# Kernel optimization log

Hardware: AMD Instinct MI355X
Metric: run time of the kernel (lower is better)

The kernel has to match this reference:

```python
import jax, jax.numpy as jnp
import numpy as np

B, N, D, H, HID = 8, 512, 512, 8, 2048


def setup_inputs() -> dict:
    key = jax.random.key(0)
    ks = jax.random.split(key, 8)
    s = 0.02
    p = lambda i, shape: jax.random.normal(ks[i], shape, jnp.float32) * s
    return dict(
        x=jax.random.normal(ks[0], (B, N, D), jnp.float32),
        Wq=p(1, (D, D)), bq=jnp.zeros((D,), jnp.float32),
        Wk=p(2, (D, D)), bk=jnp.zeros((D,), jnp.float32),
        Wv=p(3, (D, D)), bv=jnp.zeros((D,), jnp.float32),
        Wsig=p(4, (H, D)), bsig=jnp.zeros((H,), jnp.float32),
        ln1_g=jnp.ones((D,), jnp.float32), ln1_b=jnp.zeros((D,), jnp.float32),
        W1=p(5, (HID, D)), b1=jnp.zeros((HID,), jnp.float32),
        W2=p(6, (D, HID)), b2=jnp.zeros((D,), jnp.float32),
        ln2_g=jnp.ones((D,), jnp.float32), ln2_b=jnp.zeros((D,), jnp.float32),
    )


def _ln(z, g, b, eps=1e-5):
    m = jnp.mean(z, axis=-1, keepdims=True)
    v = jnp.var(z, axis=-1, keepdims=True)
    return (z - m) * jax.lax.rsqrt(v + eps) * g + b


def reference(x, Wq, bq, Wk, bk, Wv, bv, Wsig, bsig,
              ln1_g, ln1_b, W1, b1, W2, b2, ln2_g, ln2_b):
    Bb, Nn, Dd = x.shape
    Hh = bsig.shape[0]
    dh = Dd // Hh
    # --- AnomalyAttention: series attention S, Gaussian prior P, Z = S @ V ---
    Q = (x @ Wq.T + bq).reshape(Bb, Nn, Hh, dh)
    K = (x @ Wk.T + bk).reshape(Bb, Nn, Hh, dh)
    V = (x @ Wv.T + bv).reshape(Bb, Nn, Hh, dh)
    scores = jnp.einsum('bnhd,bmhd->bhnm', Q, K) / jnp.sqrt(jnp.float32(dh))
    S = jax.nn.softmax(scores, axis=-1)                       # [B,H,N,N]
    # learned positive scale sigma per (batch, position, head)
    sigma = jax.nn.softplus(x @ Wsig.T + bsig) + 1e-5         # [B,N,H]
    idx = jnp.arange(Nn, dtype=jnp.float32)
    dist2 = (idx[:, None] - idx[None, :]) ** 2                # [N,N]
    sig = jnp.transpose(sigma, (0, 2, 1))[..., None]          # [B,H,N,1]
    gauss = jnp.exp(-dist2 / (2.0 * sig * sig)) / (jnp.sqrt(2.0 * jnp.pi) * sig)
    P = gauss / jnp.sum(gauss, axis=-1, keepdims=True)        # row-normalized prior
    Zh = jnp.einsum('bhnm,bmhd->bnhd', S, V).reshape(Bb, Nn, Dd)
    # --- residual + LayerNorm + MLP(relu) + residual + LayerNorm ---
    Z = _ln(Zh + x, ln1_g, ln1_b)
    hidden = jax.nn.relu(Z @ W1.T + b1)
    x_hat = hidden @ W2.T + b2
    x_hat = _ln(x_hat + Z, ln2_g, ln2_b)
    return (x_hat, P, S)
```

## Files before the change

### kernel.cpp

```cpp
#include <hip/hip_runtime.h>
#include <cstdint>

typedef short s16x8 __attribute__((ext_vector_type(8)));
typedef float f32x4 __attribute__((ext_vector_type(4)));
using u16 = unsigned short;


__device__ __forceinline__ u16 f2bf(float f) {
    union { float f; uint32_t u; } v; v.f = f;
    uint32_t u = v.u;
    return (u16)((u + 0x7FFFu + ((u >> 16) & 1u)) >> 16);
}
__device__ __forceinline__ float bf2f(u16 u) {
    return __uint_as_float(((uint32_t)u) << 16);
}

__device__ __forceinline__ void gload_lds16(const void* g, void* l) {
    __builtin_amdgcn_global_load_lds(
        (const __attribute__((address_space(1))) unsigned int*)g,
        (__attribute__((address_space(3))) unsigned int*)l, 16, 0, 0);
}

__global__ __launch_bounds__(256) void k_convert_sigma(
    const float* __restrict__ x, const float* __restrict__ wq,
    const float* __restrict__ wk, const float* __restrict__ wv,
    const float* __restrict__ w1, const float* __restrict__ w2,
    const float* __restrict__ bq, const float* __restrict__ bk,
    const float* __restrict__ bv,
    const float* __restrict__ Wsig, const float* __restrict__ bsig,
    u16* __restrict__ xb, u16* __restrict__ wqb, u16* __restrict__ wkb,
    u16* __restrict__ wvb, u16* __restrict__ w1b, u16* __restrict__ w2b,
    float* __restrict__ biascat, float* __restrict__ sigT)
{
    int bk_ = blockIdx.x;
    int tid = threadIdx.x;
    if (bk_ >= 4866) {
        int row  = (int)(((bk_ - 4866) * 256 + tid) >> 6);
        int lane = tid & 63;
        const float4* xr = (const float4*)(x + (long)row * 512);
        float4 xa = xr[lane * 2], xc = xr[lane * 2 + 1];
        float xs[8] = {xa.x, xa.y, xa.z, xa.w, xc.x, xc.y, xc.z, xc.w};
        float ph[8];
#pragma unroll
        for (int h = 0; h < 8; ++h) {
            const float4* wr = (const float4*)(Wsig + h * 512);
            float4 wa = wr[lane * 2], wc = wr[lane * 2 + 1];
            ph[h] = xs[0]*wa.x + xs[1]*wa.y + xs[2]*wa.z + xs[3]*wa.w
                  + xs[4]*wc.x + xs[5]*wc.y + xs[6]*wc.z + xs[7]*wc.w;
        }
#pragma unroll
        for (int h = 0; h < 8; ++h)
#pragma unroll
            for (int m = 1; m < 64; m <<= 1)
                ph[h] += __shfl_xor(ph[h], m, 64);
        if (lane < 8) {
            float z  = ph[lane] + bsig[lane];
            float sp = fmaxf(z, 0.f) + log1pf(__expf(-fabsf(z)));
            int b = row >> 9, n = row & 511;
            sigT[(((long)b * 8 + lane) << 9) + n] = sp + 1e-5f;
        }
        return;
    }
    long g = (long)bk_ * 256 + tid;
    if (g >= 1245184) {
        long id = g - 1245184;
        if (id < 384) {
            const float* src = id < 128 ? bq : id < 256 ? bk : bv;
            ((float4*)biascat)[id] = ((const float4*)src)[id & 127];
        }
        return;
    }
    const float* src; u16* dst; long off;
    if      (g <  524288) { src = x;  dst = xb;  off = g; }
    else if (g <  589824) { src = wq; dst = wqb; off = g -  524288; }
    else if (g <  655360) { src = wk; dst = wkb; off = g -  589824; }
    else if (g <  720896) { src = wv; dst = wvb; off = g -  655360; }
    else if (g <  983040) { src = w1; dst = w1b; off = g -  720896; }
    else                  { src = w2; dst = w2b; off = g -  983040; }
    float4 v = ((const float4*)src)[off];
    ushort4 o;
    o.x = f2bf(v.x); o.y = f2bf(v.y); o.z = f2bf(v.z); o.w = f2bf(v.w);
    ((ushort4*)dst)[off] = o;
}

template<int BM, int BN, int EPI>
__device__ __forceinline__ void gemm_body(
    const u16* __restrict__ A, const u16* __restrict__ B,
    const float* __restrict__ bias, void* __restrict__ C,
    int lda, int ldb, int K, int bx, int by,
    u16* __restrict__ As, u16* __restrict__ Bs)
{
    constexpr int BK = 64;
    const u16* Ag = A + (long)bx * BM * lda;
    const u16* Bg = B + (long)by * BN * ldb;

    int tid  = threadIdx.x;
    int wave = tid >> 6, lane = tid & 63;
    int wm = wave >> 2, wn = wave & 3;
    constexpr int WTM = BM / 2, WTN = BN / 4;
    constexpr int FM = WTM / 16, FN = WTN / 16;
    int r16 = lane & 15, g4 = lane >> 4;

    f32x4 acc[FM][FN];
#pragma unroll
    for (int i = 0; i < FM; ++i)
#pragma unroll
        for (int j = 0; j < FN; ++j) acc[i][j] = (f32x4){0.f, 0.f, 0.f, 0.f};

    constexpr int nA = BM * BK / (512 * 8);
    constexpr int nB = BN * BK / (512 * 8);

    auto stage = [&](int buf, int k0) {
#pragma unroll
        for (int c = 0; c < nA; ++c) {
            int e = c * 512 + tid;
            int r = e >> 3, s = e & 7;
            gload_lds16(Ag + (long)r * lda + k0 + ((s ^ (r & 7)) * 8),
                        &As[buf * BM * BK + e * 8]);
        }
#pragma unroll
        for (int c = 0; c < nB; ++c) {
            int e = c * 512 + tid;
            int r = e >> 3, s = e & 7;
            gload_lds16(Bg + (long)r * ldb + k0 + ((s ^ (r & 7)) * 8),
                        &Bs[buf * BN * BK + e * 8]);
        }
    };

    stage(0, 0);
    __syncthreads();
    int cur = 0;
    const int NT = K / BK;
    for (int t = 0; t < NT; ++t) {
        if (t + 1 < NT) stage(cur ^ 1, (t + 1) * BK);
#pragma unroll
        for (int kk = 0; kk < 2; ++kk) {
            s16x8 af[FM], bfr[FN];
#pragma unroll
            for (int fm = 0; fm < FM; ++fm) {
                int row = wm * WTM + fm * 16 + r16;
                int slot = (kk * 4 + g4) ^ (row & 7);
                af[fm] = *(const s16x8*)&As[cur * BM * BK + row * 64 + slot * 8];
            }
#pragma unroll
            for (int fn = 0; fn < FN; ++fn) {
                int row = wn * WTN + fn * 16 + r16;
                int slot = (kk * 4 + g4) ^ (row & 7);
                bfr[fn] = *(const s16x8*)&Bs[cur * BN * BK + row * 64 + slot * 8];
            }
#pragma unroll
            for (int fm = 0; fm < FM; ++fm)
#pragma unroll
                for (int fn = 0; fn < FN; ++fn)
                    acc[fm][fn] = __builtin_amdgcn_mfma_f32_16x16x32_bf16(af[fm], bfr[fn], acc[fm][fn], 0, 0, 0);
        }
        __syncthreads();
        cur ^= 1;
    }

    int i0 = bx * BM + wm * WTM;
    int j0 = by * BN + wn * WTN;
#pragma unroll
    for (int fm = 0; fm < FM; ++fm)
#pragma unroll
        for (int fn = 0; fn < FN; ++fn)
#pragma unroll
            for (int j = 0; j < 4; ++j) {
                int gi = i0 + fm * 16 + (g4 << 2) + j;
                int gj = j0 + fn * 16 + r16;
                float v = acc[fm][fn][j];
                if constexpr (EPI == 3) {
                    v = fmaxf(v + bias[gj], 0.f);
                    ((u16*)C)[(long)gi * 2048 + gj] = f2bf(v);
                } else if constexpr (EPI == 4) {
                    ((float*)C)[(long)gi * 512 + gj] = v + bias[gj];
                } else {
                    v += bias[gj];
                    int mat = gj >> 9, cj = gj & 511;
                    int h = cj >> 6, d = cj & 63, b = gi >> 9, n = gi & 511;
                    u16* base = (u16*)C;
                    if (mat == 0)
                        base[(((long)(b * 8 + h) * 512 + n) << 6) + d] = f2bf(v);
                    else if (mat == 1)
                        (base + 2097152)[(((long)(b * 8 + h) * 512 + n) << 6) + d] = f2bf(v);
                    else
                        (base + 4194304)[(((long)(b * 8 + h) * 64 + d) << 9) + n] = f2bf(v);
                }
            }
}

template<int BM, int BN, int EPI>
__global__ __launch_bounds__(512) void k_gemm_nt(
    const u16* __restrict__ A, const u16* __restrict__ B,
    const float* __restrict__ bias, void* __restrict__ C,
    int lda, int ldb, int K)
{
    __shared__ __align__(16) u16 As[2 * BM * 64];
    __shared__ __align__(16) u16 Bs[2 * BN * 64];
    gemm_body<BM, BN, EPI>(A, B, bias, C, lda, ldb, K,
                           blockIdx.x, blockIdx.y, As, Bs);
}

__global__ __launch_bounds__(256) void k_attn_prior(
    const u16* __restrict__ Qb, const u16* __restrict__ Kb,
    const u16* __restrict__ Vt, const float* __restrict__ sigT,
    float* __restrict__ S, float* __restrict__ Zh, float* __restrict__ P)
{
    __shared__ __align__(16) u16 Sb[4][16][264];
    __shared__ float cmbM[2][2][16];
    __shared__ float cmbS[2][2][16];
    __shared__ float zc[2][16][66];

    int gid = blockIdx.x;
    int tid = threadIdx.x;
    int wave = tid >> 6, lane = tid & 63;

    if (gid % 9 != 0) {
        int pid = gid - gid / 9 - 1;
        int row = pid * 4 + wave;
        int n = row & 511;
        float s = sigT[row];
        float a = -1.0f / (2.0f * s * s);
        float e[8]; float sum = 0.f;
#pragma unroll
        for (int j = 0; j < 8; ++j) {
            float d = (float)(n - (lane * 8 + j));
            e[j] = __expf(a * d * d);
            sum += e[j];
        }
#pragma unroll
        for (int m = 1; m < 64; m <<= 1) sum += __shfl_xor(sum, m, 64);
        float r = 1.0f / sum;
        f32x4* dst = (f32x4*)(P + (long)row * 512 + lane * 8);
        dst[0] = (f32x4){e[0]*r, e[1]*r, e[2]*r, e[3]*r};
        dst[1] = (f32x4){e[4]*r, e[5]*r, e[6]*r, e[7]*r};
        return;
    }

    int aid = gid / 9;
    int bh = aid & 63;
    int rb = aid >> 6;
    int rg = wave >> 1, ch = wave & 1;
    int r16 = lane & 15, g4 = lane >> 4, hi8 = g4 * 8;

    int row0 = rb * 32 + rg * 16;
    const u16* Qg = Qb + ((long)bh * 512 + row0) * 64;
    const u16* Kg = Kb + ((long)bh * 512 + ch * 256) * 64;
    const u16* Vg = Vt + (long)bh * 64 * 512;

    s16x8 qa[2];
    qa[0] = *(const s16x8*)(Qg + r16 * 64 + hi8);
    qa[1] = *(const s16x8*)(Qg + r16 * 64 + 32 + hi8);

    f32x4 acc[16];
#pragma unroll
    for (int t = 0; t < 16; ++t) acc[t] = (f32x4){0.f, 0.f, 0.f, 0.f};

    __builtin_amdgcn_s_setprio(1);
#pragma unroll
    for (int kk = 0; kk < 2; ++kk)
#pragma unroll
        for (int t = 0; t < 16; ++t) {
            s16x8 b = *(const s16x8*)(Kg + (long)(t * 16 + r16) * 64 + kk * 32 + hi8);
            acc[t] = __builtin_amdgcn_mfma_f32_16x16x32_bf16(qa[kk], b, acc[t], 0, 0, 0);
        }
    __builtin_amdgcn_s_setprio(0);

    float mx[4] = {-1e30f, -1e30f, -1e30f, -1e30f};
#pragma unroll
    for (int t = 0; t < 16; ++t)
#pragma unroll
        for (int j = 0; j < 4; ++j) mx[j] = fmaxf(mx[j], acc[t][j]);
#pragma unroll
    for (int j = 0; j < 4; ++j)
#pragma unroll
        for (int m = 1; m < 16; m <<= 1) mx[j] = fmaxf(mx[j], __shfl_xor(mx[j], m, 64));

    float sm[4] = {0.f, 0.f, 0.f, 0.f};
#pragma unroll
    for (int t = 0; t < 16; ++t)
#pragma unroll
        for (int j = 0; j < 4; ++j) {
            float p = __expf(0.125f * (acc[t][j] - mx[j]));
            acc[t][j] = p;
            sm[j] += p;
        }
#pragma unroll
    for (int j = 0; j < 4; ++j)
#pragma unroll
        for (int m = 1; m < 16; m <<= 1) sm[j] += __shfl_xor(sm[j], m, 64);

    if (r16 == 0) {
#pragma unroll
        for (int j = 0; j < 4; ++j) {
            cmbM[rg][ch][g4 * 4 + j] = mx[j];
            cmbS[rg][ch][g4 * 4 + j] = sm[j];
        }
    }
    __syncthreads();

    float scale[4];
#pragma unroll
    for (int j = 0; j < 4; ++j) {
        float mo = cmbM[rg][ch ^ 1][g4 * 4 + j];
        float so = cmbS[rg][ch ^ 1][g4 * 4 + j];
        float M  = fmaxf(mx[j], mo);
        float tot = sm[j] * __expf(mx[j] - M) + so * __expf(mo - M);
        scale[j] = __expf(mx[j] - M) / tot;
    }
#pragma unroll
    for (int t = 0; t < 16; ++t)
#pragma unroll
        for (int j = 0; j < 4; ++j) acc[t][j] *= scale[j];

#pragma unroll
    for (int t = 0; t < 16; ++t)
#pragma unroll
        for (int j = 0; j < 4; ++j)
            Sb[wave][g4 * 4 + j][t * 16 + r16] = f2bf(acc[t][j]);

    f32x4 zacc[4];
#pragma unroll
    for (int fn = 0; fn < 4; ++fn) zacc[fn] = (f32x4){0.f, 0.f, 0.f, 0.f};

    __builtin_amdgcn_s_setprio(1);
#pragma unroll
    for (int kb = 0; kb < 8; ++kb) {
        s16x8 pa = *(const s16x8*)&Sb[wave][r16][kb * 32 + hi8];
#pragma unroll
        for (int fn = 0; fn < 4; ++fn) {
            s16x8 vb = *(const s16x8*)(Vg + (long)(fn * 16 + r16) * 512 + ch * 256 + kb * 32 + hi8);
            zacc[fn] = __builtin_amdgcn_mfma_f32_16x16x32_bf16(pa, vb, zacc[fn], 0, 0, 0);
        }
    }
    __builtin_amdgcn_s_setprio(0);

    long sbase = ((long)bh * 512 + row0) * 512 + ch * 256;
#pragma unroll
    for (int r = 0; r < 16; ++r) {
        ushort4 u = *(const ushort4*)&Sb[wave][r][lane * 4];
        *(f32x4*)&S[sbase + (long)r * 512 + lane * 4] =
            (f32x4){bf2f(u.x), bf2f(u.y), bf2f(u.z), bf2f(u.w)};
    }

    if (ch == 1) {
#pragma unroll
        for (int fn = 0; fn < 4; ++fn)
#pragma unroll
            for (int j = 0; j < 4; ++j)
                zc[rg][g4 * 4 + j][fn * 16 + r16] = zacc[fn][j];
    }
    __syncthreads();
    if (ch == 0) {
        long zb = ((long)(bh >> 3) * 512 + row0) * 512 + (bh & 7) * 64;
#pragma unroll
        for (int fn = 0; fn < 4; ++fn)
#pragma unroll
            for (int j = 0; j < 4; ++j)
                Zh[zb + (long)(g4 * 4 + j) * 512 + fn * 16 + r16] =
                    zacc[fn][j] + zc[rg][g4 * 4 + j][fn * 16 + r16];
    }
}

template<bool WBF>
__global__ __launch_bounds__(256) void k_ln(
    const float* __restrict__ a, const float* __restrict__ b,
    const float* __restrict__ g, const float* __restrict__ bt,
    float* __restrict__ y, u16* __restrict__ yb)
{
    int row  = (int)((blockIdx.x * 256 + threadIdx.x) >> 6);
    int lane = threadIdx.x & 63;
    const float4* ar = (const float4*)(a + (long)row * 512);
    const float4* br = (const float4*)(b + (long)row * 512);
    float4 a0 = ar[lane * 2], a1 = ar[lane * 2 + 1];
    float4 b0 = br[lane * 2], b1 = br[lane * 2 + 1];
    float v[8] = {a0.x + b0.x, a0.y + b0.y, a0.z + b0.z, a0.w + b0.w,
                  a1.x + b1.x, a1.y + b1.y, a1.z + b1.z, a1.w + b1.w};
    float s = 0.f, q = 0.f;
#pragma unroll
    for (int j = 0; j < 8; ++j) { s += v[j]; q += v[j] * v[j]; }
#pragma unroll
    for (int m = 1; m < 64; m <<= 1) {
        s += __shfl_xor(s, m, 64);
        q += __shfl_xor(q, m, 64);
    }
    float mean = s * (1.f / 512.f);
    float var  = q * (1.f / 512.f) - mean * mean;
    float rstd = rsqrtf(var + 1e-5f);
    const float4* gr = (const float4*)(g + lane * 8);
    const float4* tr = (const float4*)(bt + lane * 8);
    float4 g0 = gr[0], g1 = gr[1], t0 = tr[0], t1 = tr[1];
    float gg[8] = {g0.x, g0.y, g0.z, g0.w, g1.x, g1.y, g1.z, g1.w};
    float tt[8] = {t0.x, t0.y, t0.z, t0.w, t1.x, t1.y, t1.z, t1.w};
    float o[8];
#pragma unroll
    for (int j = 0; j < 8; ++j) o[j] = (v[j] - mean) * rstd * gg[j] + tt[j];
    float4* yr = (float4*)(y + (long)row * 512 + lane * 8);
    yr[0] = make_float4(o[0], o[1], o[2], o[3]);
    yr[1] = make_float4(o[4], o[5], o[6], o[7]);
    if constexpr (WBF) {
        s16x8 ob;
#pragma unroll
        for (int j = 0; j < 8; ++j) ob[j] = (short)f2bf(o[j]);
        *(s16x8*)(yb + (long)row * 512 + lane * 8) = ob;
    }
}

extern "C" void kernel_launch(void* const* d_in, const int* in_sizes, int n_in,
                              void* d_out, int out_size, void* d_ws, size_t ws_size,
                              hipStream_t stream)
{
    const float* x    = (const float*)d_in[0];
    const float* Wq   = (const float*)d_in[1];
    const float* bq   = (const float*)d_in[2];
    const float* Wk   = (const float*)d_in[3];
    const float* bk   = (const float*)d_in[4];
    const float* Wv   = (const float*)d_in[5];
    const float* bv   = (const float*)d_in[6];
    const float* Wsig = (const float*)d_in[7];
    const float* bsig = (const float*)d_in[8];
    const float* g1   = (const float*)d_in[9];
    const float* be1  = (const float*)d_in[10];
    const float* W1   = (const float*)d_in[11];
    const float* b1   = (const float*)d_in[12];
    const float* W2   = (const float*)d_in[13];
    const float* b2   = (const float*)d_in[14];
    const float* g2   = (const float*)d_in[15];
    const float* be2  = (const float*)d_in[16];

    float* out_xhat = (float*)d_out;
    float* out_P    = out_xhat + 2097152;
    float* out_S    = out_P + 16777216;

    char* ws = (char*)d_ws;
    u16*   xb   = (u16*)(ws + 0);
    u16*   Qb   = (u16*)(ws + 4194304);
    u16*   hid  = (u16*)(ws + 0);
    u16*   Wqb  = (u16*)(ws + 16777216);
    u16*   W1b  = (u16*)(ws + 18350080);
    u16*   W2b  = (u16*)(ws + 20447232);
    float* sigT = (float*)(ws + 22544384);
    float* Zh   = (float*)(ws + 22675456);
    float* bcat = (float*)(ws + 22675456);
    float* x2   = (float*)(ws + 22675456);
    float* Z    = (float*)(ws + 31064064);
    u16*   Zb   = (u16*)(ws + 39452672);

    u16* Wkb = Wqb + 262144;
    u16* Wvb = Wqb + 524288;

    k_convert_sigma<<<5890, 256, 0, stream>>>(x, Wq, Wk, Wv, W1, W2, bq, bk, bv,
                                              Wsig, bsig,
                                              xb, Wqb, Wkb, Wvb, W1b, W2b,
                                              bcat, sigT);

    k_gemm_nt<128,128,5><<<dim3(32,12,1),512,0,stream>>>(
        xb, Wqb, bcat, Qb, 512, 512, 512);

    k_attn_prior<<<9216, 256, 0, stream>>>(Qb, Qb + 2097152, Qb + 4194304,
                                           sigT, out_S, Zh, out_P);

    k_ln<true><<<1024,256,0,stream>>>(Zh, x, g1, be1, Z, Zb);

    k_gemm_nt<128,128,3><<<dim3(32,16,1),512,0,stream>>>(Zb, W1b, b1, hid, 512, 512, 512);

    k_gemm_nt<64,128,4><<<dim3(64,4,1),512,0,stream>>>(hid, W2b, b2, x2, 2048, 2048, 2048);

    k_ln<false><<<1024,256,0,stream>>>(x2, Z, g2, be2, out_xhat, nullptr);
}
```

Measured before the change: 142.2 us.

## Split Gaussian prior work between QKV GEMM launch and attention kernel

Half of the Gaussian prior rows are now computed by extra blocks appended to the QKV projection GEMM launch, with the other half still in the attention kernel. The attention kernel's grid shrinks and uses a simpler block-to-work mapping. The S write-back is moved before the S·V MFMA loop. The intent is to overlap memory-bound prior writes with the compute-bound GEMM and to rebalance the attention launch, at the cost of a larger combined kernel whose 512-thread prior blocks also carry the GEMM's LDS footprint.

New measurement: 133.8 us, median of 2. -5.9%, faster.

```diff
diff --git a/kernel.cpp b/kernel.cpp
--- a/kernel.cpp
+++ b/kernel.cpp
@@ -19,6 +19,27 @@
     __builtin_amdgcn_global_load_lds(
         (const __attribute__((address_space(1))) unsigned int*)g,
         (__attribute__((address_space(3))) unsigned int*)l, 16, 0, 0);
+}
+
+__device__ __forceinline__ void prior_row(
+    const float* __restrict__ sigT, float* __restrict__ P, int row, int lane)
+{
+    int n = row & 511;
+    float s = sigT[row];
+    float a = -1.0f / (2.0f * s * s);
+    float e[8]; float sum = 0.f;
+#pragma unroll
+    for (int j = 0; j < 8; ++j) {
+        float d = (float)(n - (lane * 8 + j));
+        e[j] = __expf(a * d * d);
+        sum += e[j];
+    }
+#pragma unroll
+    for (int m = 1; m < 64; m <<= 1) sum += __shfl_xor(sum, m, 64);
+    float r = 1.0f / sum;
+    f32x4* dst = (f32x4*)(P + (long)row * 512 + lane * 8);
+    dst[0] = (f32x4){e[0]*r, e[1]*r, e[2]*r, e[3]*r};
+    dst[1] = (f32x4){e[4]*r, e[5]*r, e[6]*r, e[7]*r};
 }
 
 __global__ __launch_bounds__(256) void k_convert_sigma(
@@ -83,6 +104,30 @@
     ((ushort4*)dst)[off] = o;
 }
 
+template<int EPI>
+__device__ __forceinline__ void gemm_epi(
+    const float* __restrict__ bias, void* __restrict__ C,
+    int gi, int gj, float v)
+{
+    if constexpr (EPI == 3) {
+        v = fmaxf(v + bias[gj], 0.f);
+        ((u16*)C)[(long)gi * 2048 + gj] = f2bf(v);
+    } else if constexpr (EPI == 4) {
+        ((float*)C)[(long)gi * 512 + gj] = v + bias[gj];
+    } else {
+        v += bias[gj];
+        int mat = gj >> 9, cj = gj & 511;
+        int h = cj >> 6, d = cj & 63, b = gi >> 9, n = gi & 511;
+        u16* base = (u16*)C;
+        if (mat == 0)
+            base[(((long)(b * 8 + h) * 512 + n) << 6) + d] = f2bf(v);
+        else if (mat == 1)
+            (base + 2097152)[(((long)(b * 8 + h) * 512 + n) << 6) + d] = f2bf(v);
+        else
+            (base + 4194304)[(((long)(b * 8 + h) * 64 + d) << 9) + n] = f2bf(v);
+    }
+}
+
 template<int BM, int BN, int EPI>
 __device__ __forceinline__ void gemm_body(
     const u16* __restrict__ A, const u16* __restrict__ B,
@@ -165,28 +210,10 @@
 #pragma unroll
         for (int fn = 0; fn < FN; ++fn)
 #pragma unroll
-            for (int j = 0; j < 4; ++j) {
-                int gi = i0 + fm * 16 + (g4 << 2) + j;
-                int gj = j0 + fn * 16 + r16;
-                float v = acc[fm][fn][j];
-                if constexpr (EPI == 3) {
-                    v = fmaxf(v + bias[gj], 0.f);
-                    ((u16*)C)[(long)gi * 2048 + gj] = f2bf(v);
-                } else if constexpr (EPI == 4) {
-                    ((float*)C)[(long)gi * 512 + gj] = v + bias[gj];
-                } else {
-                    v += bias[gj];
-                    int mat = gj >> 9, cj = gj & 511;
-                    int h = cj >> 6, d = cj & 63, b = gi >> 9, n = gi & 511;
-                    u16* base = (u16*)C;
-                    if (mat == 0)
-                        base[(((long)(b * 8 + h) * 512 + n) << 6) + d] = f2bf(v);
-                    else if (mat == 1)
-                        (base + 2097152)[(((long)(b * 8 + h) * 512 + n) << 6) + d] = f2bf(v);
-                    else
-                        (base + 4194304)[(((long)(b * 8 + h) * 64 + d) << 9) + n] = f2bf(v);
-                }
-            }
+            for (int j = 0; j < 4; ++j)
+                gemm_epi<EPI>(bias, C,
+                              i0 + fm * 16 + (g4 << 2) + j,
+                              j0 + fn * 16 + r16, acc[fm][fn][j]);
 }
 
 template<int BM, int BN, int EPI>
@@ -201,6 +228,24 @@
                            blockIdx.x, blockIdx.y, As, Bs);
 }
 
+__global__ __launch_bounds__(512) void k_qkv_prior(
+    const u16* __restrict__ A, const u16* __restrict__ B,
+    const float* __restrict__ bias, void* __restrict__ C,
+    const float* __restrict__ sigT, float* __restrict__ P)
+{
+    __shared__ __align__(16) u16 As[2 * 128 * 64];
+    __shared__ __align__(16) u16 Bs[2 * 128 * 64];
+    int gid = blockIdx.x;
+    if (gid < 384) {
+        gemm_body<128, 128, 5>(A, B, bias, C, 512, 512, 512,
+                               gid % 32, gid / 32, As, Bs);
+        return;
+    }
+    int pid  = gid - 384;
+    int wave = threadIdx.x >> 6, lane = threadIdx.x & 63;
+    prior_row(sigT, P, 16384 + pid * 8 + wave, lane);
+}
+
 __global__ __launch_bounds__(256) void k_attn_prior(
     const u16* __restrict__ Qb, const u16* __restrict__ Kb,
     const u16* __restrict__ Vt, const float* __restrict__ sigT,
@@ -215,31 +260,13 @@
     int tid = threadIdx.x;
     int wave = tid >> 6, lane = tid & 63;
 
-    if (gid % 9 != 0) {
-        int pid = gid - gid / 9 - 1;
-        int row = pid * 4 + wave;
-        int n = row & 511;
-        float s = sigT[row];
-        float a = -1.0f / (2.0f * s * s);
-        float e[8]; float sum = 0.f;
-#pragma unroll
-        for (int j = 0; j < 8; ++j) {
-            float d = (float)(n - (lane * 8 + j));
-            e[j] = __expf(a * d * d);
-            sum += e[j];
-        }
-#pragma unroll
-        for (int m = 1; m < 64; m <<= 1) sum += __shfl_xor(sum, m, 64);
-        float r = 1.0f / sum;
-        f32x4* dst = (f32x4*)(P + (long)row * 512 + lane * 8);
-        dst[0] = (f32x4){e[0]*r, e[1]*r, e[2]*r, e[3]*r};
-        dst[1] = (f32x4){e[4]*r, e[5]*r, e[6]*r, e[7]*r};
+    if (gid >= 1024) {
+        prior_row(sigT, P, (gid - 1024) * 4 + wave, lane);
         return;
     }
 
-    int aid = gid / 9;
-    int bh = aid & 63;
-    int rb = aid >> 6;
+    int bh = gid & 63;
+    int rb = gid >> 6;
     int rg = wave >> 1, ch = wave & 1;
     int r16 = lane & 15, g4 = lane >> 4, hi8 = g4 * 8;
 
@@ -319,22 +346,6 @@
         for (int j = 0; j < 4; ++j)
             Sb[wave][g4 * 4 + j][t * 16 + r16] = f2bf(acc[t][j]);
 
-    f32x4 zacc[4];
-#pragma unroll
-    for (int fn = 0; fn < 4; ++fn) zacc[fn] = (f32x4){0.f, 0.f, 0.f, 0.f};
-
-    __builtin_amdgcn_s_setprio(1);
-#pragma unroll
-    for (int kb = 0; kb < 8; ++kb) {
-        s16x8 pa = *(const s16x8*)&Sb[wave][r16][kb * 32 + hi8];
-#pragma unroll
-        for (int fn = 0; fn < 4; ++fn) {
-            s16x8 vb = *(const s16x8*)(Vg + (long)(fn * 16 + r16) * 512 + ch * 256 + kb * 32 + hi8);
-            zacc[fn] = __builtin_amdgcn_mfma_f32_16x16x32_bf16(pa, vb, zacc[fn], 0, 0, 0);
-        }
-    }
-    __builtin_amdgcn_s_setprio(0);
-
     long sbase = ((long)bh * 512 + row0) * 512 + ch * 256;
 #pragma unroll
     for (int r = 0; r < 16; ++r) {
@@ -342,6 +353,22 @@
         *(f32x4*)&S[sbase + (long)r * 512 + lane * 4] =
             (f32x4){bf2f(u.x), bf2f(u.y), bf2f(u.z), bf2f(u.w)};
     }
+
+    f32x4 zacc[4];
+#pragma unroll
+    for (int fn = 0; fn < 4; ++fn) zacc[fn] = (f32x4){0.f, 0.f, 0.f, 0.f};
+
+    __builtin_amdgcn_s_setprio(1);
+#pragma unroll
+    for (int kb = 0; kb < 8; ++kb) {
+        s16x8 pa = *(const s16x8*)&Sb[wave][r16][kb * 32 + hi8];
+#pragma unroll
+        for (int fn = 0; fn < 4; ++fn) {
+            s16x8 vb = *(const s16x8*)(Vg + (long)(fn * 16 + r16) * 512 + ch * 256 + kb * 32 + hi8);
+            zacc[fn] = __builtin_amdgcn_mfma_f32_16x16x32_bf16(pa, vb, zacc[fn], 0, 0, 0);
+        }
+    }
+    __builtin_amdgcn_s_setprio(0);
 
     if (ch == 1) {
 #pragma unroll
@@ -454,10 +481,9 @@
                                               xb, Wqb, Wkb, Wvb, W1b, W2b,
                                               bcat, sigT);
 
-    k_gemm_nt<128,128,5><<<dim3(32,12,1),512,0,stream>>>(
-        xb, Wqb, bcat, Qb, 512, 512, 512);
-
-    k_attn_prior<<<9216, 256, 0, stream>>>(Qb, Qb + 2097152, Qb + 4194304,
+    k_qkv_prior<<<2432, 512, 0, stream>>>(xb, Wqb, bcat, Qb, sigT, out_P);
+
+    k_attn_prior<<<5120, 256, 0, stream>>>(Qb, Qb + 2097152, Qb + 4194304,
                                            sigT, out_S, Zh, out_P);
 
     k_ln<true><<<1024,256,0,stream>>>(Zh, x, g1, be1, Z, Zb);
```
